# Kernel tuning notes

Measured on AMD Instinct MI355X. Metric: run time of the kernel, lower is better.

Reference implementation:

```python
import jax, jax.numpy as jnp
import numpy as np

LN_EPS = 1e-5
KERNEL_EPS = 1e-4


def layer_norm(x, gamma, beta):
    mu = jnp.mean(x, axis=-1, keepdims=True)
    var = jnp.mean((x - mu) ** 2, axis=-1, keepdims=True)
    return (x - mu) * jax.lax.rsqrt(var + LN_EPS) * gamma + beta


def softmax_kernel(data, proj, is_query):
    # Performer softmax random-feature map (performer-pytorch softmax_kernel)
    d = data.shape[-1]
    m = proj.shape[0]
    data_normalizer = d ** -0.25
    ratio = m ** -0.5
    # [B,H,S,D] x [M,D] -> [B,H,S,M]
    proj_data = jnp.einsum('bhnd,md->bhnm', data_normalizer * data, proj)
    diag = 0.5 * (data_normalizer ** 2) * jnp.sum(data * data, axis=-1, keepdims=True)
    if is_query:
        mx = jax.lax.stop_gradient(jnp.max(proj_data, axis=-1, keepdims=True))
    else:
        mx = jax.lax.stop_gradient(jnp.max(proj_data, axis=(-2, -1), keepdims=True))
    return ratio * (jnp.exp(proj_data - diag - mx) + KERNEL_EPS)


def setup_inputs() -> dict:
    key = jax.random.key(0)
    k1, k2 = jax.random.split(key)
    B, S, D, M, H = 4, 4096, 256, 256, 8
    x = jax.random.normal(k1, (B, S, D), dtype=jnp.float32)
    gamma = jnp.ones((D,), dtype=jnp.float32)
    beta = jnp.zeros((D,), dtype=jnp.float32)
    proj_matrix = jax.random.normal(k2, (M, D), dtype=jnp.float32)
    return {"x": x, "gamma": gamma, "beta": beta, "proj_matrix": proj_matrix, "num_heads": H}


def reference(x, gamma, beta, proj_matrix, num_heads):
    xn = layer_norm(x, gamma, beta)                       # [B,S,D]
    B, S, D = xn.shape
    h = jnp.broadcast_to(xn[:, None], (B, num_heads, S, D))  # stacked copies per head
    q = softmax_kernel(h, proj_matrix, True)              # [B,H,S,M]
    k = softmax_kernel(h, proj_matrix, False)             # [B,H,S,M]
    v = h                                                 # [B,H,S,D]
    # non-causal linear attention
    k_sum = jnp.sum(k, axis=-2)                           # [B,H,M]
    d_inv = 1.0 / jnp.einsum('bhnm,bhm->bhn', q, k_sum)   # [B,H,S]
    context = jnp.einsum('bhnm,bhnd->bhmd', k, v)         # [B,H,M,D]
    out = jnp.einsum('bhmd,bhnm,bhn->bhnd', context, q, d_inv)
    return out
```

## Files before the change

kernel.cpp:

```cpp
#include <hip/hip_runtime.h>
#include <math.h>

#define Bn 4
#define Hn 8
#define Sn 4096
#define Dn 256
#define Mn 256
#define BSn (Bn*Sn)
#define LN_EPS 1e-5f
#define KEPS 1e-4f
#define DATA_NORM 0.25f
#define RATIO 0.0625f

typedef short s8v __attribute__((ext_vector_type(8)));
typedef short s4v __attribute__((ext_vector_type(4)));
typedef float f4v __attribute__((ext_vector_type(4)));

#define BSTR 72

__device__ __forceinline__ unsigned short f2bf(float x) {
    unsigned u = __float_as_uint(x);
    u += 0x7FFFu + ((u >> 16) & 1u);
    return (unsigned short)(u >> 16);
}
__device__ __forceinline__ float bf2f(unsigned short h) {
    return __uint_as_float(((unsigned)h) << 16);
}
__device__ __forceinline__ unsigned enc_f(float f) {
    unsigned u = __float_as_uint(f);
    return (u & 0x80000000u) ? ~u : (u | 0x80000000u);
}
__device__ __forceinline__ float dec_f(unsigned u) {
    unsigned b = (u & 0x80000000u) ? (u ^ 0x80000000u) : ~u;
    return __uint_as_float(b);
}

__global__ __launch_bounds__(256) void k_ln(const float* __restrict__ X,
                                            const float* __restrict__ gamma,
                                            const float* __restrict__ beta,
                                            const float* __restrict__ P,
                                            unsigned short* __restrict__ XNh,
                                            unsigned short* __restrict__ XNl,
                                            unsigned short* __restrict__ Ph,
                                            unsigned short* __restrict__ Pl,
                                            float* __restrict__ diag,
                                            unsigned* __restrict__ mxqI,
                                            float* __restrict__ KSUM,
                                            unsigned* __restrict__ mxkI) {
    if (blockIdx.x >= BSn / 4) {
        const int e = blockIdx.x - BSn / 4;
        if (e < 32) {
            const int i = (e * 256 + threadIdx.x) * 8;
            float v[8];
            *(float4*)&v[0] = *(const float4*)&P[i];
            *(float4*)&v[4] = *(const float4*)&P[i + 4];
            s8v hh, ll;
            #pragma unroll
            for (int q = 0; q < 8; q++) {
                unsigned short h = f2bf(v[q]);
                hh[q] = (short)h;
                ll[q] = (short)f2bf(v[q] - bf2f(h));
            }
            *(s8v*)&Ph[i] = hh;
            *(s8v*)&Pl[i] = ll;
        } else {
            KSUM[threadIdx.x]       = 0.0f;
            KSUM[threadIdx.x + 256] = 0.0f;
            KSUM[threadIdx.x + 512] = 0.0f;
            KSUM[threadIdx.x + 768] = 0.0f;
            if (threadIdx.x < 4) mxkI[threadIdx.x] = 0u;
        }
        return;
    }
    const int w = threadIdx.x >> 6, l = threadIdx.x & 63;
    const int row = blockIdx.x * 4 + w;
    float4 x = *(const float4*)&X[(size_t)row * Dn + l * 4];
    float s = x.x + x.y + x.z + x.w;
    #pragma unroll
    for (int o = 32; o > 0; o >>= 1) s += __shfl_xor(s, o);
    const float mean = s * (1.0f / Dn);
    float xn[4] = {x.x - mean, x.y - mean, x.z - mean, x.w - mean};
    float vs = xn[0] * xn[0] + xn[1] * xn[1] + xn[2] * xn[2] + xn[3] * xn[3];
    #pragma unroll
    for (int o = 32; o > 0; o >>= 1) vs += __shfl_xor(vs, o);
    const float rs = rsqrtf(vs * (1.0f / Dn) + LN_EPS);
    float4 g = *(const float4*)&gamma[l * 4];
    float4 bt = *(const float4*)&beta[l * 4];
    xn[0] = xn[0] * rs * g.x + bt.x;
    xn[1] = xn[1] * rs * g.y + bt.y;
    xn[2] = xn[2] * rs * g.z + bt.z;
    xn[3] = xn[3] * rs * g.w + bt.w;
    s4v hv, lv;
    float d2 = 0.0f;
    #pragma unroll
    for (int c = 0; c < 4; c++) {
        d2 += xn[c] * xn[c];
        unsigned short h = f2bf(xn[c]);
        hv[c] = (short)h;
        lv[c] = (short)f2bf(xn[c] - bf2f(h));
    }
    *(s4v*)&XNh[(size_t)row * Dn + l * 4] = hv;
    *(s4v*)&XNl[(size_t)row * Dn + l * 4] = lv;
    #pragma unroll
    for (int o = 32; o > 0; o >>= 1) d2 += __shfl_xor(d2, o);
    if (l == 0) { diag[row] = 0.03125f * d2; mxqI[row] = 0u; }
}

__global__ __launch_bounds__(256, 2) void k_gemm1(const unsigned short* __restrict__ XNh,
                                                  const unsigned short* __restrict__ XNl,
                                                  const unsigned short* __restrict__ Ph,
                                                  const unsigned short* __restrict__ Pl,
                                                  float* __restrict__ PD,
                                                  unsigned* __restrict__ mxqI,
                                                  unsigned* __restrict__ mxkI) {
    __shared__ unsigned short Ah[64 * BSTR], Al[64 * BSTR];
    __shared__ unsigned short Bh[128 * BSTR], Bl[128 * BSTR];
    __shared__ float bmS[4];
    const int t = threadIdx.x, lane = t & 63, w = t >> 6;
    const int wr = w >> 1, wc = w & 1, quad = lane >> 4, cc = lane & 15;
    const int r0 = blockIdx.x * 64, m0 = blockIdx.y * 128;
    const int ar0 = t >> 3, ac8 = (t & 7) * 8;
    f4v acc[2][4];
    #pragma unroll
    for (int i = 0; i < 2; i++)
        #pragma unroll
        for (int j = 0; j < 4; j++)
            #pragma unroll
            for (int r = 0; r < 4; r++) acc[i][j][r] = 0.0f;

    for (int kt = 0; kt < Dn; kt += 64) {
        __syncthreads();
        *(s8v*)&Ah[ar0 * BSTR + ac8]        = *(const s8v*)&XNh[(size_t)(r0 + ar0) * Dn + kt + ac8];
        *(s8v*)&Al[ar0 * BSTR + ac8]        = *(const s8v*)&XNl[(size_t)(r0 + ar0) * Dn + kt + ac8];
        *(s8v*)&Ah[(ar0 + 32) * BSTR + ac8] = *(const s8v*)&XNh[(size_t)(r0 + ar0 + 32) * Dn + kt + ac8];
        *(s8v*)&Al[(ar0 + 32) * BSTR + ac8] = *(const s8v*)&XNl[(size_t)(r0 + ar0 + 32) * Dn + kt + ac8];
        #pragma unroll
        for (int ss = 0; ss < 4; ss++) {
            const int row = ar0 + ss * 32;
            *(s8v*)&Bh[row * BSTR + ac8] = *(const s8v*)&Ph[(size_t)(m0 + row) * Dn + kt + ac8];
            *(s8v*)&Bl[row * BSTR + ac8] = *(const s8v*)&Pl[(size_t)(m0 + row) * Dn + kt + ac8];
        }
        __syncthreads();
        #pragma unroll
        for (int ks = 0; ks < 2; ks++) {
            s8v ah[2], al[2], bh[4], bl[4];
            #pragma unroll
            for (int i = 0; i < 2; i++) {
                const int m = wr * 32 + i * 16 + cc;
                ah[i] = *(const s8v*)&Ah[m * BSTR + ks * 32 + quad * 8];
                al[i] = *(const s8v*)&Al[m * BSTR + ks * 32 + quad * 8];
            }
            #pragma unroll
            for (int j = 0; j < 4; j++) {
                const int n = wc * 64 + j * 16 + cc;
                bh[j] = *(const s8v*)&Bh[n * BSTR + ks * 32 + quad * 8];
                bl[j] = *(const s8v*)&Bl[n * BSTR + ks * 32 + quad * 8];
            }
            #pragma unroll
            for (int i = 0; i < 2; i++)
                #pragma unroll
                for (int j = 0; j < 4; j++) {
                    acc[i][j] = __builtin_amdgcn_mfma_f32_16x16x32_bf16(ah[i], bh[j], acc[i][j], 0, 0, 0);
                    acc[i][j] = __builtin_amdgcn_mfma_f32_16x16x32_bf16(ah[i], bl[j], acc[i][j], 0, 0, 0);
                    acc[i][j] = __builtin_amdgcn_mfma_f32_16x16x32_bf16(al[i], bh[j], acc[i][j], 0, 0, 0);
                }
        }
    }
    float rmax[2][4];
    #pragma unroll
    for (int i = 0; i < 2; i++)
        #pragma unroll
        for (int r = 0; r < 4; r++) rmax[i][r] = -INFINITY;
    #pragma unroll
    for (int i = 0; i < 2; i++) {
        const int row = r0 + wr * 32 + i * 16 + quad * 4;
        #pragma unroll
        for (int j = 0; j < 4; j++) {
            const int col = m0 + wc * 64 + j * 16 + cc;
            #pragma unroll
            for (int r = 0; r < 4; r++) {
                float v = DATA_NORM * acc[i][j][r];
                PD[(size_t)(row + r) * Mn + col] = v;
                rmax[i][r] = fmaxf(rmax[i][r], v);
            }
        }
    }
    #pragma unroll
    for (int i = 0; i < 2; i++)
        #pragma unroll
        for (int r = 0; r < 4; r++) {
            float v = rmax[i][r];
            v = fmaxf(v, __shfl_xor(v, 1));
            v = fmaxf(v, __shfl_xor(v, 2));
            v = fmaxf(v, __shfl_xor(v, 4));
            v = fmaxf(v, __shfl_xor(v, 8));
            if (cc == 0)
                atomicMax(&mxqI[r0 + wr * 32 + i * 16 + quad * 4 + r], enc_f(v));
        }
    float bm = fmaxf(fmaxf(rmax[0][0], rmax[0][1]), fmaxf(rmax[0][2], rmax[0][3]));
    bm = fmaxf(bm, fmaxf(fmaxf(rmax[1][0], rmax[1][1]), fmaxf(rmax[1][2], rmax[1][3])));
    #pragma unroll
    for (int o = 32; o > 0; o >>= 1) bm = fmaxf(bm, __shfl_xor(bm, o));
    if (lane == 0) bmS[w] = bm;
    __syncthreads();
    if (t == 0)
        atomicMax(&mxkI[r0 >> 12], enc_f(fmaxf(fmaxf(bmS[0], bmS[1]), fmaxf(bmS[2], bmS[3]))));
}

__global__ __launch_bounds__(256) void k_featvt(const float* __restrict__ PD,
                                                const unsigned short* __restrict__ XNh,
                                                const float* __restrict__ diag,
                                                const unsigned* __restrict__ mxkI,
                                                const unsigned* __restrict__ mxqI,
                                                unsigned short* __restrict__ KT,
                                                unsigned short* __restrict__ QR,
                                                unsigned short* __restrict__ VT,
                                                float* __restrict__ KSUM) {
    const int s0 = blockIdx.x * 64, c0 = blockIdx.y * 64, z = blockIdx.z;
    const int t = threadIdx.x;
    const int sr = t >> 2, cc16 = (t & 3) * 16;
    if (z < 4) {
        __shared__ float T[64][65];
        const int b = z;
        const int gr = b * Sn + s0 + sr;
        const float mk = dec_f(mxkI[b]);
        const float dmv = diag[gr] + mk;
        const float srow = __expf(mk - dec_f(mxqI[gr]));
        const float* p = PD + (size_t)gr * Mn + c0 + cc16;
        float v[16];
        *(float4*)&v[0]  = *(const float4*)&p[0];
        *(float4*)&v[4]  = *(const float4*)&p[4];
        *(float4*)&v[8]  = *(const float4*)&p[8];
        *(float4*)&v[12] = *(const float4*)&p[12];
        s8v q0, q1;
        #pragma unroll
        for (int e = 0; e < 16; e++) {
            float ev = __expf(v[e] - dmv);
            T[cc16 + e][sr] = RATIO * (ev + KEPS);
            unsigned short qb = f2bf(RATIO * (ev * srow + KEPS));
            if (e < 8) q0[e] = (short)qb; else q1[e - 8] = (short)qb;
        }
        *(s8v*)&QR[(size_t)gr * Mn + c0 + cc16]     = q0;
        *(s8v*)&QR[(size_t)gr * Mn + c0 + cc16 + 8] = q1;
        __syncthreads();
        const int ml = t >> 2, sc = (t & 3) * 16;
        float ks = 0.0f;
        s8v o0, o1;
        #pragma unroll
        for (int i = 0; i < 8; i++) {
            float f0 = T[ml][sc + i], f1 = T[ml][sc + 8 + i];
            ks += f0 + f1;
            o0[i] = (short)f2bf(f0);
            o1[i] = (short)f2bf(f1);
        }
        unsigned short* q = KT + ((size_t)b * Mn + c0 + ml) * Sn + s0 + sc;
        *(s8v*)&q[0] = o0;
        *(s8v*)&q[8] = o1;
        ks += __shfl_xor(ks, 1);
        ks += __shfl_xor(ks, 2);
        if ((t & 3) == 0) atomicAdd(&KSUM[b * Mn + c0 + ml], ks);
    } else {
        __shared__ unsigned short Tu[64][72];
        const int b = z - 4;
        const int gr = b * Sn + s0 + sr;
        const unsigned short* p = XNh + (size_t)gr * Dn + c0 + cc16;
        s8v x0 = *(const s8v*)&p[0], x1 = *(const s8v*)&p[8];
        #pragma unroll
        for (int e = 0; e < 8; e++) {
            Tu[cc16 + e][sr]     = (unsigned short)x0[e];
            Tu[cc16 + 8 + e][sr] = (unsigned short)x1[e];
        }
        __syncthreads();
        const int dl = t >> 2, sc = (t & 3) * 16;
        s8v o0, o1;
        #pragma unroll
        for (int i = 0; i < 8; i++) {
            o0[i] = (short)Tu[dl][sc + i];
            o1[i] = (short)Tu[dl][sc + 8 + i];
        }
        unsigned short* q = VT + ((size_t)b * Dn + c0 + dl) * Sn + s0 + sc;
        *(s8v*)&q[0] = o0;
        *(s8v*)&q[8] = o1;
    }
}

__global__ __launch_bounds__(256, 2) void k_gemm2(const unsigned short* __restrict__ VT,
                                                  const unsigned short* __restrict__ KT,
                                                  float* __restrict__ PART) {
    __shared__ unsigned short Abuf[64 * BSTR], Bbuf[64 * BSTR];
    const int t = threadIdx.x, lane = t & 63, w = t >> 6;
    const int wr = w >> 1, wc = w & 1, quad = lane >> 4, cc = lane & 15;
    const int chunk = blockIdx.x, til = blockIdx.y, b = blockIdx.z;
    const int d0 = (til >> 2) * 64, m0 = (til & 3) * 64;
    const unsigned short* Ab = VT + ((size_t)b * Dn + d0) * Sn + chunk * 1024;
    const unsigned short* Bb = KT + ((size_t)b * Mn + m0) * Sn + chunk * 1024;
    const int sr = t >> 2, sc = (t & 3) * 16;
    f4v acc[2][2];
    #pragma unroll
    for (int i = 0; i < 2; i++)
        #pragma unroll
        for (int j = 0; j < 2; j++)
            #pragma unroll
            for (int r = 0; r < 4; r++) acc[i][j][r] = 0.0f;

    for (int kt = 0; kt < 1024; kt += 64) {
        __syncthreads();
        *(s8v*)&Abuf[sr * BSTR + sc]     = *(const s8v*)&Ab[(size_t)sr * Sn + kt + sc];
        *(s8v*)&Abuf[sr * BSTR + sc + 8] = *(const s8v*)&Ab[(size_t)sr * Sn + kt + sc + 8];
        *(s8v*)&Bbuf[sr * BSTR + sc]     = *(const s8v*)&Bb[(size_t)sr * Sn + kt + sc];
        *(s8v*)&Bbuf[sr * BSTR + sc + 8] = *(const s8v*)&Bb[(size_t)sr * Sn + kt + sc + 8];
        __syncthreads();
        #pragma unroll
        for (int ks = 0; ks < 2; ks++) {
            s8v a[2], bb[2];
            #pragma unroll
            for (int i = 0; i < 2; i++)
                a[i] = *(const s8v*)&Abuf[(wr * 32 + i * 16 + cc) * BSTR + ks * 32 + quad * 8];
            #pragma unroll
            for (int j = 0; j < 2; j++)
                bb[j] = *(const s8v*)&Bbuf[(wc * 32 + j * 16 + cc) * BSTR + ks * 32 + quad * 8];
            #pragma unroll
            for (int i = 0; i < 2; i++)
                #pragma unroll
                for (int j = 0; j < 2; j++)
                    acc[i][j] = __builtin_amdgcn_mfma_f32_16x16x32_bf16(a[i], bb[j], acc[i][j], 0, 0, 0);
        }
    }
    float* dst = PART + (size_t)(chunk * Bn + b) * (Dn * Mn);
    #pragma unroll
    for (int i = 0; i < 2; i++) {
        const int drow = d0 + wr * 32 + i * 16 + quad * 4;
        #pragma unroll
        for (int j = 0; j < 2; j++) {
            const int col = m0 + wc * 32 + j * 16 + cc;
            #pragma unroll
            for (int r = 0; r < 4; r++)
                dst[(size_t)(drow + r) * Mn + col] = acc[i][j][r];
        }
    }
}

__global__ __launch_bounds__(256) void k_ctxred(const float* __restrict__ PART,
                                                unsigned short* __restrict__ CT) {
    const int g = blockIdx.x * 256 + threadIdx.x;
    float4 s = make_float4(0.f, 0.f, 0.f, 0.f);
    #pragma unroll
    for (int c = 0; c < 4; c++) {
        float4 p = *(const float4*)&PART[(size_t)c * 262144 + (size_t)g * 4];
        s.x += p.x; s.y += p.y; s.z += p.z; s.w += p.w;
    }
    s4v o;
    o[0] = (short)f2bf(s.x); o[1] = (short)f2bf(s.y);
    o[2] = (short)f2bf(s.z); o[3] = (short)f2bf(s.w);
    *(s4v*)&CT[(size_t)g * 4] = o;
}

__global__ __launch_bounds__(256, 2) void k_gemm3(const unsigned short* __restrict__ QR,
                                                  const unsigned short* __restrict__ CT,
                                                  const float* __restrict__ KSUM,
                                                  float* __restrict__ OUT) {
    __shared__ unsigned short Abuf[64 * BSTR], Bbuf[128 * BSTR];
    __shared__ float kslds[Mn];
    __shared__ float dinvS[64];
    __shared__ float OutS[64][136];
    const int t = threadIdx.x, lane = t & 63, w = t >> 6;
    const int wr = w >> 1, wc = w & 1, quad = lane >> 4, cc = lane & 15;
    const int r0 = blockIdx.x * 64, d0 = blockIdx.y * 128;
    const int b = r0 >> 12;
    kslds[t] = KSUM[b * Mn + t];
    const int ar0 = t >> 3, ac8 = (t & 7) * 8;
    float qks0 = 0.0f, qks1 = 0.0f;
    f4v acc[2][4];
    #pragma unroll
    for (int i = 0; i < 2; i++)
        #pragma unroll
        for (int j = 0; j < 4; j++)
            #pragma unroll
            for (int r = 0; r < 4; r++) acc[i][j][r] = 0.0f;

    for (int kt = 0; kt < Mn; kt += 64) {
        __syncthreads();
        s8v a0 = *(const s8v*)&QR[(size_t)(r0 + ar0) * Mn + kt + ac8];
        s8v a1 = *(const s8v*)&QR[(size_t)(r0 + ar0 + 32) * Mn + kt + ac8];
        *(s8v*)&Abuf[ar0 * BSTR + ac8]        = a0;
        *(s8v*)&Abuf[(ar0 + 32) * BSTR + ac8] = a1;
        #pragma unroll
        for (int e = 0; e < 8; e++) {
            const float ks = kslds[kt + ac8 + e];
            qks0 += bf2f((unsigned short)a0[e]) * ks;
            qks1 += bf2f((unsigned short)a1[e]) * ks;
        }
        #pragma unroll
        for (int ss = 0; ss < 4; ss++) {
            const int row = ar0 + ss * 32;
            *(s8v*)&Bbuf[row * BSTR + ac8] =
                *(const s8v*)&CT[((size_t)b * Dn + d0 + row) * Mn + kt + ac8];
        }
        __syncthreads();
        #pragma unroll
        for (int ks = 0; ks < 2; ks++) {
            s8v a[2], bb[4];
            #pragma unroll
            for (int i = 0; i < 2; i++)
                a[i] = *(const s8v*)&Abuf[(wr * 32 + i * 16 + cc) * BSTR + ks * 32 + quad * 8];
            #pragma unroll
            for (int j = 0; j < 4; j++)
                bb[j] = *(const s8v*)&Bbuf[(wc * 64 + j * 16 + cc) * BSTR + ks * 32 + quad * 8];
            #pragma unroll
            for (int i = 0; i < 2; i++)
                #pragma unroll
                for (int j = 0; j < 4; j++)
                    acc[i][j] = __builtin_amdgcn_mfma_f32_16x16x32_bf16(a[i], bb[j], acc[i][j], 0, 0, 0);
        }
    }
    qks0 += __shfl_xor(qks0, 1); qks0 += __shfl_xor(qks0, 2); qks0 += __shfl_xor(qks0, 4);
    qks1 += __shfl_xor(qks1, 1); qks1 += __shfl_xor(qks1, 2); qks1 += __shfl_xor(qks1, 4);
    if ((t & 7) == 0) {
        dinvS[ar0]      = 1.0f / qks0;
        dinvS[ar0 + 32] = 1.0f / qks1;
    }
    __syncthreads();
    #pragma unroll
    for (int i = 0; i < 2; i++) {
        const int rl0 = wr * 32 + i * 16 + quad * 4;
        #pragma unroll
        for (int r = 0; r < 4; r++) {
            const float dv = dinvS[rl0 + r];
            #pragma unroll
            for (int j = 0; j < 4; j++)
                OutS[rl0 + r][wc * 64 + j * 16 + cc] = acc[i][j][r] * dv;
        }
    }
    __syncthreads();
    const int rb = t >> 5;
    const int c4 = (t & 31) * 4;
    #pragma unroll
    for (int it = 0; it < 8; it++) {
        const int row = it * 8 + rb;
        float4 v = *(const float4*)&OutS[row][c4];
        const int gr = r0 + row;
        const int ss = gr & (Sn - 1);
        const size_t basep = ((size_t)(b * Hn) * Sn + ss) * Dn + d0 + c4;
        #pragma unroll
        for (int h = 0; h < Hn; h++)
            *(float4*)&OUT[basep + (size_t)h * Sn * Dn] = v;
    }
}

extern "C" void kernel_launch(void* const* d_in, const int* in_sizes, int n_in,
                              void* d_out, int out_size, void* d_ws, size_t ws_size,
                              hipStream_t stream) {
    const float* X     = (const float*)d_in[0];
    const float* gamma = (const float*)d_in[1];
    const float* beta  = (const float*)d_in[2];
    const float* P     = (const float*)d_in[3];
    float* OUT = (float*)d_out;

    char* base = (char*)d_ws;
    unsigned short* XNh = (unsigned short*)(base);
    unsigned short* XNl = (unsigned short*)(base + 8388608);
    float*          PD  = (float*)(base + 16777216);
    unsigned short* QR  = (unsigned short*)(base + 33554432);
    unsigned short* VT  = (unsigned short*)(base + 41943040);
    unsigned short* CT  = (unsigned short*)(base + 50331648);
    unsigned short* Ph  = (unsigned short*)(base + 50855936);
    unsigned short* Pl  = (unsigned short*)(base + 50987008);
    float*          diag = (float*)(base + 51118080);
    unsigned*       mxqI = (unsigned*)(base + 51183616);
    unsigned*       mxkI = (unsigned*)(base + 51314688);
    float*          KSUM = (float*)(base + 51314944);
    unsigned short* KT   = XNl;
    float*          PART = PD;

    k_ln<<<BSn / 4 + 33, 256, 0, stream>>>(X, gamma, beta, P, XNh, XNl, Ph, Pl, diag, mxqI, KSUM, mxkI);
    k_gemm1<<<dim3(BSn / 64, Mn / 128), 256, 0, stream>>>(XNh, XNl, Ph, Pl, PD, mxqI, mxkI);
    k_featvt<<<dim3(Sn / 64, 4, 8), 256, 0, stream>>>(PD, XNh, diag, mxkI, mxqI, KT, QR, VT, KSUM);
    k_gemm2<<<dim3(4, 16, Bn), 256, 0, stream>>>(VT, KT, PART);
    k_ctxred<<<256, 256, 0, stream>>>(PART, CT);
    k_gemm3<<<dim3(BSn / 64, Dn / 128), 256, 0, stream>>>(QR, CT, KSUM, OUT);
}
```

Baseline: 205.0 us.

## Recompute LayerNorm on the fly in consumers instead of storing split bf16 XN

LayerNorm now writes only per-row mean and rstd. k_gemm1 and k_featvt reload the raw fp32 input, normalize it while staging, and build the hi/lo bf16 split in shared memory, so the XNh/XNl buffers are gone. This removes 16 MB of writes and their later reads. In exchange, fp32 X (twice the bytes of one bf16 copy) is read twice by gemm1 (once per M tile) and again by featvt, and the staging path does more ALU work. The workspace layout is repacked, and KT now gets its own region instead of aliasing XNl.

```diff
diff --git a/kernel.cpp b/kernel.cpp
--- a/kernel.cpp
+++ b/kernel.cpp
@@ -39,12 +39,11 @@
                                             const float* __restrict__ gamma,
                                             const float* __restrict__ beta,
                                             const float* __restrict__ P,
-                                            unsigned short* __restrict__ XNh,
-                                            unsigned short* __restrict__ XNl,
+                                            float2* __restrict__ stats,
+                                            float* __restrict__ diag,
+                                            unsigned* __restrict__ mxqI,
                                             unsigned short* __restrict__ Ph,
                                             unsigned short* __restrict__ Pl,
-                                            float* __restrict__ diag,
-                                            unsigned* __restrict__ mxqI,
                                             float* __restrict__ KSUM,
                                             unsigned* __restrict__ mxkI) {
     if (blockIdx.x >= BSn / 4) {
@@ -90,24 +89,20 @@
     xn[1] = xn[1] * rs * g.y + bt.y;
     xn[2] = xn[2] * rs * g.z + bt.z;
     xn[3] = xn[3] * rs * g.w + bt.w;
-    s4v hv, lv;
-    float d2 = 0.0f;
-    #pragma unroll
-    for (int c = 0; c < 4; c++) {
-        d2 += xn[c] * xn[c];
-        unsigned short h = f2bf(xn[c]);
-        hv[c] = (short)h;
-        lv[c] = (short)f2bf(xn[c] - bf2f(h));
-    }
-    *(s4v*)&XNh[(size_t)row * Dn + l * 4] = hv;
-    *(s4v*)&XNl[(size_t)row * Dn + l * 4] = lv;
+    float d2 = xn[0] * xn[0] + xn[1] * xn[1] + xn[2] * xn[2] + xn[3] * xn[3];
     #pragma unroll
     for (int o = 32; o > 0; o >>= 1) d2 += __shfl_xor(d2, o);
-    if (l == 0) { diag[row] = 0.03125f * d2; mxqI[row] = 0u; }
-}
-
-__global__ __launch_bounds__(256, 2) void k_gemm1(const unsigned short* __restrict__ XNh,
-                                                  const unsigned short* __restrict__ XNl,
+    if (l == 0) {
+        stats[row] = make_float2(mean, rs);
+        diag[row] = 0.03125f * d2;
+        mxqI[row] = 0u;
+    }
+}
+
+__global__ __launch_bounds__(256, 2) void k_gemm1(const float* __restrict__ X,
+                                                  const float2* __restrict__ stats,
+                                                  const float* __restrict__ gamma,
+                                                  const float* __restrict__ beta,
                                                   const unsigned short* __restrict__ Ph,
                                                   const unsigned short* __restrict__ Pl,
                                                   float* __restrict__ PD,
@@ -120,6 +115,8 @@
     const int wr = w >> 1, wc = w & 1, quad = lane >> 4, cc = lane & 15;
     const int r0 = blockIdx.x * 64, m0 = blockIdx.y * 128;
     const int ar0 = t >> 3, ac8 = (t & 7) * 8;
+    const float2 st0 = stats[r0 + ar0];
+    const float2 st1 = stats[r0 + ar0 + 32];
     f4v acc[2][4];
     #pragma unroll
     for (int i = 0; i < 2; i++)
@@ -130,10 +127,31 @@
 
     for (int kt = 0; kt < Dn; kt += 64) {
         __syncthreads();
-        *(s8v*)&Ah[ar0 * BSTR + ac8]        = *(const s8v*)&XNh[(size_t)(r0 + ar0) * Dn + kt + ac8];
-        *(s8v*)&Al[ar0 * BSTR + ac8]        = *(const s8v*)&XNl[(size_t)(r0 + ar0) * Dn + kt + ac8];
-        *(s8v*)&Ah[(ar0 + 32) * BSTR + ac8] = *(const s8v*)&XNh[(size_t)(r0 + ar0 + 32) * Dn + kt + ac8];
-        *(s8v*)&Al[(ar0 + 32) * BSTR + ac8] = *(const s8v*)&XNl[(size_t)(r0 + ar0 + 32) * Dn + kt + ac8];
+        {
+            float g8[8], b8[8];
+            *(float4*)&g8[0] = *(const float4*)&gamma[kt + ac8];
+            *(float4*)&g8[4] = *(const float4*)&gamma[kt + ac8 + 4];
+            *(float4*)&b8[0] = *(const float4*)&beta[kt + ac8];
+            *(float4*)&b8[4] = *(const float4*)&beta[kt + ac8 + 4];
+            #pragma unroll
+            for (int rr = 0; rr < 2; rr++) {
+                const int row = r0 + ar0 + rr * 32;
+                const float2 st = rr ? st1 : st0;
+                float xv[8];
+                *(float4*)&xv[0] = *(const float4*)&X[(size_t)row * Dn + kt + ac8];
+                *(float4*)&xv[4] = *(const float4*)&X[(size_t)row * Dn + kt + ac8 + 4];
+                s8v hv, lv;
+                #pragma unroll
+                for (int e = 0; e < 8; e++) {
+                    float xn = (xv[e] - st.x) * st.y * g8[e] + b8[e];
+                    unsigned short h = f2bf(xn);
+                    hv[e] = (short)h;
+                    lv[e] = (short)f2bf(xn - bf2f(h));
+                }
+                *(s8v*)&Ah[(ar0 + rr * 32) * BSTR + ac8] = hv;
+                *(s8v*)&Al[(ar0 + rr * 32) * BSTR + ac8] = lv;
+            }
+        }
         #pragma unroll
         for (int ss = 0; ss < 4; ss++) {
             const int row = ar0 + ss * 32;
@@ -208,7 +226,10 @@
 }
 
 __global__ __launch_bounds__(256) void k_featvt(const float* __restrict__ PD,
-                                                const unsigned short* __restrict__ XNh,
+                                                const float* __restrict__ X,
+                                                const float2* __restrict__ stats,
+                                                const float* __restrict__ gamma,
+                                                const float* __restrict__ beta,
                                                 const float* __restrict__ diag,
                                                 const unsigned* __restrict__ mxkI,
                                                 const unsigned* __restrict__ mxqI,
@@ -263,12 +284,25 @@
         __shared__ unsigned short Tu[64][72];
         const int b = z - 4;
         const int gr = b * Sn + s0 + sr;
-        const unsigned short* p = XNh + (size_t)gr * Dn + c0 + cc16;
-        s8v x0 = *(const s8v*)&p[0], x1 = *(const s8v*)&p[8];
-        #pragma unroll
-        for (int e = 0; e < 8; e++) {
-            Tu[cc16 + e][sr]     = (unsigned short)x0[e];
-            Tu[cc16 + 8 + e][sr] = (unsigned short)x1[e];
+        const float2 st = stats[gr];
+        const float* xp = X + (size_t)gr * Dn + c0 + cc16;
+        float xv[16], g16[16], b16[16];
+        *(float4*)&xv[0]  = *(const float4*)&xp[0];
+        *(float4*)&xv[4]  = *(const float4*)&xp[4];
+        *(float4*)&xv[8]  = *(const float4*)&xp[8];
+        *(float4*)&xv[12] = *(const float4*)&xp[12];
+        *(float4*)&g16[0]  = *(const float4*)&gamma[c0 + cc16];
+        *(float4*)&g16[4]  = *(const float4*)&gamma[c0 + cc16 + 4];
+        *(float4*)&g16[8]  = *(const float4*)&gamma[c0 + cc16 + 8];
+        *(float4*)&g16[12] = *(const float4*)&gamma[c0 + cc16 + 12];
+        *(float4*)&b16[0]  = *(const float4*)&beta[c0 + cc16];
+        *(float4*)&b16[4]  = *(const float4*)&beta[c0 + cc16 + 4];
+        *(float4*)&b16[8]  = *(const float4*)&beta[c0 + cc16 + 8];
+        *(float4*)&b16[12] = *(const float4*)&beta[c0 + cc16 + 12];
+        #pragma unroll
+        for (int e = 0; e < 16; e++) {
+            float xn = (xv[e] - st.x) * st.y * g16[e] + b16[e];
+            Tu[cc16 + e][sr] = f2bf(xn);
         }
         __syncthreads();
         const int dl = t >> 2, sc = (t & 3) * 16;
@@ -457,24 +491,23 @@
     float* OUT = (float*)d_out;
 
     char* base = (char*)d_ws;
-    unsigned short* XNh = (unsigned short*)(base);
-    unsigned short* XNl = (unsigned short*)(base + 8388608);
-    float*          PD  = (float*)(base + 16777216);
-    unsigned short* QR  = (unsigned short*)(base + 33554432);
-    unsigned short* VT  = (unsigned short*)(base + 41943040);
-    unsigned short* CT  = (unsigned short*)(base + 50331648);
-    unsigned short* Ph  = (unsigned short*)(base + 50855936);
-    unsigned short* Pl  = (unsigned short*)(base + 50987008);
-    float*          diag = (float*)(base + 51118080);
-    unsigned*       mxqI = (unsigned*)(base + 51183616);
-    unsigned*       mxkI = (unsigned*)(base + 51314688);
-    float*          KSUM = (float*)(base + 51314944);
-    unsigned short* KT   = XNl;
+    float*          PD   = (float*)(base);
+    unsigned short* QR   = (unsigned short*)(base + 16777216);
+    unsigned short* VT   = (unsigned short*)(base + 25165824);
+    unsigned short* KT   = (unsigned short*)(base + 33554432);
+    unsigned short* CT   = (unsigned short*)(base + 41943040);
+    unsigned short* Ph   = (unsigned short*)(base + 42467328);
+    unsigned short* Pl   = (unsigned short*)(base + 42598400);
+    float2*         stats= (float2*)(base + 42729472);
+    float*          diag = (float*)(base + 42860544);
+    unsigned*       mxqI = (unsigned*)(base + 42926080);
+    unsigned*       mxkI = (unsigned*)(base + 42991616);
+    float*          KSUM = (float*)(base + 42991680);
     float*          PART = PD;
 
-    k_ln<<<BSn / 4 + 33, 256, 0, stream>>>(X, gamma, beta, P, XNh, XNl, Ph, Pl, diag, mxqI, KSUM, mxkI);
-    k_gemm1<<<dim3(BSn / 64, Mn / 128), 256, 0, stream>>>(XNh, XNl, Ph, Pl, PD, mxqI, mxkI);
-    k_featvt<<<dim3(Sn / 64, 4, 8), 256, 0, stream>>>(PD, XNh, diag, mxkI, mxqI, KT, QR, VT, KSUM);
+    k_ln<<<BSn / 4 + 33, 256, 0, stream>>>(X, gamma, beta, P, stats, diag, mxqI, Ph, Pl, KSUM, mxkI);
+    k_gemm1<<<dim3(BSn / 64, Mn / 128), 256, 0, stream>>>(X, stats, gamma, beta, Ph, Pl, PD, mxqI, mxkI);
+    k_featvt<<<dim3(Sn / 64, 4, 8), 256, 0, stream>>>(PD, X, stats, gamma, beta, diag, mxkI, mxqI, KT, QR, VT, KSUM);
     k_gemm2<<<dim3(4, 16, Bn), 256, 0, stream>>>(VT, KT, PART);
     k_ctxred<<<256, 256, 0, stream>>>(PART, CT);
     k_gemm3<<<dim3(BSn / 64, Dn / 128), 256, 0, stream>>>(QR, CT, KSUM, OUT);
```

After: 207.5 us. About the same (+1.2%).

## Fuse V transpose into context GEMM via swizzled LDS loads, split S into 8 chunks

Applied to the files above, without the earlier changes.

Removes the separate VT transpose branch from the feature kernel. The context GEMM now loads row-major normalized X directly and transposes it into LDS with an XOR swizzle to avoid bank conflicts. The S dimension is split into 8 chunks of 512 instead of 4 of 1024, which doubles the GEMM grid for more parallelism, and the reduction kernel now sums 8 partials. The cost is scattered 2-byte LDS stores in the GEMM load phase and twice the partial-sum traffic.

```diff
diff --git a/kernel.cpp b/kernel.cpp
--- a/kernel.cpp
+++ b/kernel.cpp
@@ -208,83 +208,56 @@
 }
 
 __global__ __launch_bounds__(256) void k_featvt(const float* __restrict__ PD,
-                                                const unsigned short* __restrict__ XNh,
                                                 const float* __restrict__ diag,
                                                 const unsigned* __restrict__ mxkI,
                                                 const unsigned* __restrict__ mxqI,
                                                 unsigned short* __restrict__ KT,
                                                 unsigned short* __restrict__ QR,
-                                                unsigned short* __restrict__ VT,
                                                 float* __restrict__ KSUM) {
-    const int s0 = blockIdx.x * 64, c0 = blockIdx.y * 64, z = blockIdx.z;
+    const int s0 = blockIdx.x * 64, c0 = blockIdx.y * 64, b = blockIdx.z;
     const int t = threadIdx.x;
     const int sr = t >> 2, cc16 = (t & 3) * 16;
-    if (z < 4) {
-        __shared__ float T[64][65];
-        const int b = z;
-        const int gr = b * Sn + s0 + sr;
-        const float mk = dec_f(mxkI[b]);
-        const float dmv = diag[gr] + mk;
-        const float srow = __expf(mk - dec_f(mxqI[gr]));
-        const float* p = PD + (size_t)gr * Mn + c0 + cc16;
-        float v[16];
-        *(float4*)&v[0]  = *(const float4*)&p[0];
-        *(float4*)&v[4]  = *(const float4*)&p[4];
-        *(float4*)&v[8]  = *(const float4*)&p[8];
-        *(float4*)&v[12] = *(const float4*)&p[12];
-        s8v q0, q1;
-        #pragma unroll
-        for (int e = 0; e < 16; e++) {
-            float ev = __expf(v[e] - dmv);
-            T[cc16 + e][sr] = RATIO * (ev + KEPS);
-            unsigned short qb = f2bf(RATIO * (ev * srow + KEPS));
-            if (e < 8) q0[e] = (short)qb; else q1[e - 8] = (short)qb;
-        }
-        *(s8v*)&QR[(size_t)gr * Mn + c0 + cc16]     = q0;
-        *(s8v*)&QR[(size_t)gr * Mn + c0 + cc16 + 8] = q1;
-        __syncthreads();
-        const int ml = t >> 2, sc = (t & 3) * 16;
-        float ks = 0.0f;
-        s8v o0, o1;
-        #pragma unroll
-        for (int i = 0; i < 8; i++) {
-            float f0 = T[ml][sc + i], f1 = T[ml][sc + 8 + i];
-            ks += f0 + f1;
-            o0[i] = (short)f2bf(f0);
-            o1[i] = (short)f2bf(f1);
-        }
-        unsigned short* q = KT + ((size_t)b * Mn + c0 + ml) * Sn + s0 + sc;
-        *(s8v*)&q[0] = o0;
-        *(s8v*)&q[8] = o1;
-        ks += __shfl_xor(ks, 1);
-        ks += __shfl_xor(ks, 2);
-        if ((t & 3) == 0) atomicAdd(&KSUM[b * Mn + c0 + ml], ks);
-    } else {
-        __shared__ unsigned short Tu[64][72];
-        const int b = z - 4;
-        const int gr = b * Sn + s0 + sr;
-        const unsigned short* p = XNh + (size_t)gr * Dn + c0 + cc16;
-        s8v x0 = *(const s8v*)&p[0], x1 = *(const s8v*)&p[8];
-        #pragma unroll
-        for (int e = 0; e < 8; e++) {
-            Tu[cc16 + e][sr]     = (unsigned short)x0[e];
-            Tu[cc16 + 8 + e][sr] = (unsigned short)x1[e];
-        }
-        __syncthreads();
-        const int dl = t >> 2, sc = (t & 3) * 16;
-        s8v o0, o1;
-        #pragma unroll
-        for (int i = 0; i < 8; i++) {
-            o0[i] = (short)Tu[dl][sc + i];
-            o1[i] = (short)Tu[dl][sc + 8 + i];
-        }
-        unsigned short* q = VT + ((size_t)b * Dn + c0 + dl) * Sn + s0 + sc;
-        *(s8v*)&q[0] = o0;
-        *(s8v*)&q[8] = o1;
-    }
-}
-
-__global__ __launch_bounds__(256, 2) void k_gemm2(const unsigned short* __restrict__ VT,
+    __shared__ float T[64][65];
+    const int gr = b * Sn + s0 + sr;
+    const float mk = dec_f(mxkI[b]);
+    const float dmv = diag[gr] + mk;
+    const float srow = __expf(mk - dec_f(mxqI[gr]));
+    const float* p = PD + (size_t)gr * Mn + c0 + cc16;
+    float v[16];
+    *(float4*)&v[0]  = *(const float4*)&p[0];
+    *(float4*)&v[4]  = *(const float4*)&p[4];
+    *(float4*)&v[8]  = *(const float4*)&p[8];
+    *(float4*)&v[12] = *(const float4*)&p[12];
+    s8v q0, q1;
+    #pragma unroll
+    for (int e = 0; e < 16; e++) {
+        float ev = __expf(v[e] - dmv);
+        T[cc16 + e][sr] = RATIO * (ev + KEPS);
+        unsigned short qb = f2bf(RATIO * (ev * srow + KEPS));
+        if (e < 8) q0[e] = (short)qb; else q1[e - 8] = (short)qb;
+    }
+    *(s8v*)&QR[(size_t)gr * Mn + c0 + cc16]     = q0;
+    *(s8v*)&QR[(size_t)gr * Mn + c0 + cc16 + 8] = q1;
+    __syncthreads();
+    const int ml = t >> 2, sc = (t & 3) * 16;
+    float ks = 0.0f;
+    s8v o0, o1;
+    #pragma unroll
+    for (int i = 0; i < 8; i++) {
+        float f0 = T[ml][sc + i], f1 = T[ml][sc + 8 + i];
+        ks += f0 + f1;
+        o0[i] = (short)f2bf(f0);
+        o1[i] = (short)f2bf(f1);
+    }
+    unsigned short* q = KT + ((size_t)b * Mn + c0 + ml) * Sn + s0 + sc;
+    *(s8v*)&q[0] = o0;
+    *(s8v*)&q[8] = o1;
+    ks += __shfl_xor(ks, 1);
+    ks += __shfl_xor(ks, 2);
+    if ((t & 3) == 0) atomicAdd(&KSUM[b * Mn + c0 + ml], ks);
+}
+
+__global__ __launch_bounds__(256, 2) void k_gemm2(const unsigned short* __restrict__ XNh,
                                                   const unsigned short* __restrict__ KT,
                                                   float* __restrict__ PART) {
     __shared__ unsigned short Abuf[64 * BSTR], Bbuf[64 * BSTR];
@@ -292,9 +265,8 @@
     const int wr = w >> 1, wc = w & 1, quad = lane >> 4, cc = lane & 15;
     const int chunk = blockIdx.x, til = blockIdx.y, b = blockIdx.z;
     const int d0 = (til >> 2) * 64, m0 = (til & 3) * 64;
-    const unsigned short* Ab = VT + ((size_t)b * Dn + d0) * Sn + chunk * 1024;
-    const unsigned short* Bb = KT + ((size_t)b * Mn + m0) * Sn + chunk * 1024;
     const int sr = t >> 2, sc = (t & 3) * 16;
+    const int dc = (t & 3) * 16;
     f4v acc[2][2];
     #pragma unroll
     for (int i = 0; i < 2; i++)
@@ -303,19 +275,37 @@
             #pragma unroll
             for (int r = 0; r < 4; r++) acc[i][j][r] = 0.0f;
 
-    for (int kt = 0; kt < 1024; kt += 64) {
-        __syncthreads();
-        *(s8v*)&Abuf[sr * BSTR + sc]     = *(const s8v*)&Ab[(size_t)sr * Sn + kt + sc];
-        *(s8v*)&Abuf[sr * BSTR + sc + 8] = *(const s8v*)&Ab[(size_t)sr * Sn + kt + sc + 8];
-        *(s8v*)&Bbuf[sr * BSTR + sc]     = *(const s8v*)&Bb[(size_t)sr * Sn + kt + sc];
-        *(s8v*)&Bbuf[sr * BSTR + sc + 8] = *(const s8v*)&Bb[(size_t)sr * Sn + kt + sc + 8];
+    int aswz[2];
+    #pragma unroll
+    for (int i = 0; i < 2; i++)
+        aswz[i] = ((((wr * 32 + i * 16 + cc) >> 3) & 7) << 3);
+
+    for (int kt = 0; kt < 512; kt += 64) {
+        __syncthreads();
+        {
+            const int gs = chunk * 512 + kt + sr;
+            const unsigned short* xp = &XNh[((size_t)b * Sn + gs) * Dn + d0 + dc];
+            s8v x0 = *(const s8v*)&xp[0];
+            s8v x1 = *(const s8v*)&xp[8];
+            #pragma unroll
+            for (int e = 0; e < 8; e++) {
+                const int dl0 = dc + e, dl1 = dc + 8 + e;
+                Abuf[dl0 * BSTR + (sr ^ (((dl0 >> 3) & 7) << 3))] = (unsigned short)x0[e];
+                Abuf[dl1 * BSTR + (sr ^ (((dl1 >> 3) & 7) << 3))] = (unsigned short)x1[e];
+            }
+        }
+        {
+            const unsigned short* bp = &KT[((size_t)b * Mn + m0 + sr) * Sn + chunk * 512 + kt + sc];
+            *(s8v*)&Bbuf[sr * BSTR + sc]     = *(const s8v*)&bp[0];
+            *(s8v*)&Bbuf[sr * BSTR + sc + 8] = *(const s8v*)&bp[8];
+        }
         __syncthreads();
         #pragma unroll
         for (int ks = 0; ks < 2; ks++) {
             s8v a[2], bb[2];
             #pragma unroll
             for (int i = 0; i < 2; i++)
-                a[i] = *(const s8v*)&Abuf[(wr * 32 + i * 16 + cc) * BSTR + ks * 32 + quad * 8];
+                a[i] = *(const s8v*)&Abuf[(wr * 32 + i * 16 + cc) * BSTR + ((ks * 32 + quad * 8) ^ aswz[i])];
             #pragma unroll
             for (int j = 0; j < 2; j++)
                 bb[j] = *(const s8v*)&Bbuf[(wc * 32 + j * 16 + cc) * BSTR + ks * 32 + quad * 8];
@@ -345,7 +335,7 @@
     const int g = blockIdx.x * 256 + threadIdx.x;
     float4 s = make_float4(0.f, 0.f, 0.f, 0.f);
     #pragma unroll
-    for (int c = 0; c < 4; c++) {
+    for (int c = 0; c < 8; c++) {
         float4 p = *(const float4*)&PART[(size_t)c * 262144 + (size_t)g * 4];
         s.x += p.x; s.y += p.y; s.z += p.z; s.w += p.w;
     }
@@ -461,21 +451,20 @@
     unsigned short* XNl = (unsigned short*)(base + 8388608);
     float*          PD  = (float*)(base + 16777216);
     unsigned short* QR  = (unsigned short*)(base + 33554432);
-    unsigned short* VT  = (unsigned short*)(base + 41943040);
-    unsigned short* CT  = (unsigned short*)(base + 50331648);
-    unsigned short* Ph  = (unsigned short*)(base + 50855936);
-    unsigned short* Pl  = (unsigned short*)(base + 50987008);
-    float*          diag = (float*)(base + 51118080);
-    unsigned*       mxqI = (unsigned*)(base + 51183616);
-    unsigned*       mxkI = (unsigned*)(base + 51314688);
-    float*          KSUM = (float*)(base + 51314944);
+    unsigned short* CT  = (unsigned short*)(base + 41943040);
+    unsigned short* Ph  = (unsigned short*)(base + 42467328);
+    unsigned short* Pl  = (unsigned short*)(base + 42598400);
+    float*          diag = (float*)(base + 42729472);
+    unsigned*       mxqI = (unsigned*)(base + 42795008);
+    unsigned*       mxkI = (unsigned*)(base + 42860544);
+    float*          KSUM = (float*)(base + 42860608);
     unsigned short* KT   = XNl;
     float*          PART = PD;
 
     k_ln<<<BSn / 4 + 33, 256, 0, stream>>>(X, gamma, beta, P, XNh, XNl, Ph, Pl, diag, mxqI, KSUM, mxkI);
     k_gemm1<<<dim3(BSn / 64, Mn / 128), 256, 0, stream>>>(XNh, XNl, Ph, Pl, PD, mxqI, mxkI);
-    k_featvt<<<dim3(Sn / 64, 4, 8), 256, 0, stream>>>(PD, XNh, diag, mxkI, mxqI, KT, QR, VT, KSUM);
-    k_gemm2<<<dim3(4, 16, Bn), 256, 0, stream>>>(VT, KT, PART);
+    k_featvt<<<dim3(Sn / 64, 4, 4), 256, 0, stream>>>(PD, diag, mxkI, mxqI, KT, QR, KSUM);
+    k_gemm2<<<dim3(8, 16, Bn), 256, 0, stream>>>(XNh, KT, PART);
     k_ctxred<<<256, 256, 0, stream>>>(PART, CT);
     k_gemm3<<<dim3(BSn / 64, Dn / 128), 256, 0, stream>>>(QR, CT, KSUM, OUT);
 }
```

New measurement: 201.1 us. No clear change (-1.9%).
